# Optimization experiments

Hardware: AMD Instinct MI355X
Metric: run time of the kernel (lower is better)

## Reference

```python
import jax, jax.numpy as jnp
import numpy as np

NUM_HEADS = 4
SPLIT_SIZE = 8  # idx == 1 -> H_sp = H, W_sp = split_size (vertical stripe windows)


def setup_inputs() -> dict:
    key = jax.random.key(0)
    k1, k2, k3 = jax.random.split(key, 3)
    temp = jax.random.normal(k1, (16, 3, 128, 64, 64), dtype=jnp.float32)
    conv_w = jax.random.normal(k2, (128, 1, 3, 3), dtype=jnp.float32) * 0.1  # depthwise LePE conv
    conv_b = jax.random.normal(k3, (128,), dtype=jnp.float32) * 0.1
    return {"temp": temp, "conv_w": conv_w, "conv_b": conv_b}


def reference(temp, conv_w, conv_b):
    B, _, C, H, W = temp.shape
    H_sp, W_sp = H, SPLIT_SIZE          # idx == 1 cross-shaped window
    # H % H_sp == 0 and W % W_sp == 0 -> F.pad amounts are zero here
    nH, nW = H // H_sp, W // W_sp
    L = H_sp * W_sp                     # tokens per window
    hd = C // NUM_HEADS
    scale = hd ** -0.5

    q, k, v = temp[:, 0], temp[:, 1], temp[:, 2]  # each [B, C, H, W]

    def im2cswin(x):
        # img2windows: B C H W -> (B*nH*nW, L, C) then split heads -> (Bw, nh, L, hd)
        x = x.reshape(B, C, nH, H_sp, nW, W_sp).transpose(0, 2, 4, 3, 5, 1)
        x = x.reshape(-1, L, NUM_HEADS, hd).transpose(0, 2, 1, 3)
        return x

    qw = im2cswin(q) * scale            # (Bw, nh, L, hd)
    kw = im2cswin(k)

    # get_rpe: window-partition v as images, depthwise 3x3 conv for LePE
    vimg = v.reshape(B, C, nH, H_sp, nW, W_sp).transpose(0, 2, 4, 1, 3, 5)
    vimg = vimg.reshape(-1, C, H_sp, W_sp)  # (Bw, C, H_sp, W_sp)
    rpe = jax.lax.conv_general_dilated(
        vimg, conv_w, window_strides=(1, 1), padding="SAME",
        dimension_numbers=("NCHW", "OIHW", "NCHW"), feature_group_count=C,
    ) + conv_b[None, :, None, None]
    rpe = rpe.reshape(-1, NUM_HEADS, hd, L).transpose(0, 1, 3, 2)  # (Bw, nh, L, hd)
    vw = vimg.reshape(-1, NUM_HEADS, hd, L).transpose(0, 1, 3, 2)

    attn = jax.nn.softmax(jnp.einsum("wnld,wnmd->wnlm", qw, kw), axis=-1)
    out = jnp.einsum("wnlm,wnmd->wnld", attn, vw) + rpe  # (Bw, nh, L, hd)

    out = out.transpose(0, 2, 1, 3).reshape(-1, L, C)    # (Bw, L, C)
    # windows2img: (Bw, L, C) -> (B, H, W, C)
    out = out.reshape(B, nH, nW, H_sp, W_sp, C).transpose(0, 1, 3, 2, 4, 5)
    out = out.reshape(B, H, W, C)
    return out.reshape(B, H * W, C)
```

## Files before the change

### kernel.cpp

```cpp
#include <hip/hip_runtime.h>

typedef __attribute__((ext_vector_type(8))) short short8;
typedef __attribute__((ext_vector_type(2))) float float2_t;
typedef __attribute__((ext_vector_type(4))) float float4_t;
typedef __attribute__((ext_vector_type(4))) int int4_t;
typedef __attribute__((ext_vector_type(2))) unsigned uint2_t;

#define CH_STRIDE 4096
#define IMG_STRIDE 524288
#define HW 4096
#define V520 520

static __device__ __forceinline__ short f2b(float x) {
    unsigned u = __builtin_bit_cast(unsigned, x);
    u = (u + 0x7fffu + ((u >> 16) & 1u)) >> 16;
    return (short)u;
}
static __device__ __forceinline__ float bitsf(unsigned u) { return __builtin_bit_cast(float, u); }
static __device__ __forceinline__ unsigned bitsu(float f) { return __builtin_bit_cast(unsigned, f); }

__global__ __launch_bounds__(1024) void cswin_fused(
    const float* __restrict__ temp, const float* __restrict__ cw,
    const float* __restrict__ cb, float* __restrict__ out)
{
    __shared__ short Kc[64 * 40];
    __shared__ short Vt[32 * V520];

    int bx = blockIdx.x;
    int nw = bx >> 6;
    int r  = bx & 63;
    int b  = r >> 2;
    int n  = r & 3;

    int t    = threadIdx.x;
    int wv   = t >> 6;
    int lane = t & 63;
    int mr   = lane & 15;
    int q    = lane >> 4;

    const float* tq = temp + (size_t)b * 3 * IMG_STRIDE + (size_t)(n * 32) * CH_STRIDE + nw * 8;
    const float* tk = tq + IMG_STRIDE;
    const float* tv = tk + IMG_STRIDE;

    int row0 = wv * 32;
    const float qscale = 0.2550348889072310f;

    short8 Qf[2];
    #pragma unroll
    for (int qt = 0; qt < 2; ++qt) {
        int l = row0 + qt * 16 + mr;
        int sp = (l >> 3) * 64 + (l & 7);
        short8 f;
        #pragma unroll
        for (int j = 0; j < 8; ++j)
            f[j] = f2b(tq[(q * 8 + j) * CH_STRIDE + sp] * qscale);
        Qf[qt] = f;
    }

    float4_t zero4 = {0.f, 0.f, 0.f, 0.f};
    float4_t acc[2][2];
    #pragma unroll
    for (int dt = 0; dt < 2; ++dt)
        #pragma unroll
        for (int qt = 0; qt < 2; ++qt)
            acc[dt][qt] = zero4;
    float lsum[2] = {0.f, 0.f};

    int ld  = t >> 5;
    int seg = t & 31;
    const float* tkld = tk + (size_t)ld * CH_STRIDE;
    const float* tvld = tv + (size_t)ld * CH_STRIDE;

    float kx[2], vx[2];
    #pragma unroll
    for (int i = 0; i < 2; ++i) {
        int lb = seg + 32 * i;
        int sp = (lb >> 3) * 64 + (lb & 7);
        kx[i] = tkld[sp]; vx[i] = tvld[sp];
    }
    {
        #pragma unroll
        for (int i = 0; i < 2; ++i) {
            int kl = seg + 32 * i;
            Kc[kl * 40 + ld] = f2b(kx[i]);
            Vt[ld * V520 + kl] = f2b(vx[i]);
        }
    }
    #pragma unroll
    for (int i = 0; i < 2; ++i) {
        int lb = 64 + seg + 32 * i;
        int sp = (lb >> 3) * 64 + (lb & 7);
        kx[i] = tkld[sp]; vx[i] = tvld[sp];
    }

    #pragma unroll 1
    for (int ch = 0; ch < 8; ++ch) {
        __syncthreads();

        #pragma unroll
        for (int g = 0; g < 2; ++g) {
            short8 KaA = *reinterpret_cast<const short8*>(&Kc[((2 * g) * 16 + mr) * 40 + q * 8]);
            short8 KaB = *reinterpret_cast<const short8*>(&Kc[((2 * g + 1) * 16 + mr) * 40 + q * 8]);
            unsigned pa0[2], pa1[2], pb0[2], pb1[2];
            #pragma unroll
            for (int qt = 0; qt < 2; ++qt) {
                float4_t sA = __builtin_amdgcn_mfma_f32_16x16x32_bf16(KaA, Qf[qt], zero4, 0, 0, 0);
                float4_t sB = __builtin_amdgcn_mfma_f32_16x16x32_bf16(KaB, Qf[qt], zero4, 0, 0, 0);
                float eA0 = __builtin_amdgcn_exp2f(sA.x), eA1 = __builtin_amdgcn_exp2f(sA.y);
                float eA2 = __builtin_amdgcn_exp2f(sA.z), eA3 = __builtin_amdgcn_exp2f(sA.w);
                float eB0 = __builtin_amdgcn_exp2f(sB.x), eB1 = __builtin_amdgcn_exp2f(sB.y);
                float eB2 = __builtin_amdgcn_exp2f(sB.z), eB3 = __builtin_amdgcn_exp2f(sB.w);
                lsum[qt] += ((eA0 + eA1) + (eA2 + eA3)) + ((eB0 + eB1) + (eB2 + eB3));
                pa0[qt] = __builtin_amdgcn_perm(bitsu(eA1), bitsu(eA0), 0x07060302u);
                pa1[qt] = __builtin_amdgcn_perm(bitsu(eA3), bitsu(eA2), 0x07060302u);
                pb0[qt] = __builtin_amdgcn_perm(bitsu(eB1), bitsu(eB0), 0x07060302u);
                pb1[qt] = __builtin_amdgcn_perm(bitsu(eB3), bitsu(eB2), 0x07060302u);
            }
            int base = ch * 64 + g * 32 + q * 8;
            short8 Va0 = *reinterpret_cast<const short8*>(&Vt[mr * V520 + base]);
            short8 Va1 = *reinterpret_cast<const short8*>(&Vt[(16 + mr) * V520 + base]);
            #pragma unroll
            for (int qt = 0; qt < 2; ++qt) {
                uint2_t re = __builtin_amdgcn_permlane32_swap(pa0[qt], pb0[qt], 0, 0);
                uint2_t we = __builtin_amdgcn_permlane16_swap(re.x, re.y, 0, 0);
                uint2_t ro = __builtin_amdgcn_permlane32_swap(pa1[qt], pb1[qt], 0, 0);
                uint2_t wo = __builtin_amdgcn_permlane16_swap(ro.x, ro.y, 0, 0);
                int4_t pi = { (int)we.x, (int)wo.x, (int)we.y, (int)wo.y };
                short8 Pb = __builtin_bit_cast(short8, pi);
                acc[0][qt] = __builtin_amdgcn_mfma_f32_16x16x32_bf16(Va0, Pb, acc[0][qt], 0, 0, 0);
                acc[1][qt] = __builtin_amdgcn_mfma_f32_16x16x32_bf16(Va1, Pb, acc[1][qt], 0, 0, 0);
            }
        }

        if (ch < 7) {
            __syncthreads();
            #pragma unroll
            for (int i = 0; i < 2; ++i) {
                int kl = seg + 32 * i;
                Kc[kl * 40 + ld] = f2b(kx[i]);
                Vt[ld * V520 + (ch + 1) * 64 + kl] = f2b(vx[i]);
            }
            if (ch < 6) {
                #pragma unroll
                for (int i = 0; i < 2; ++i) {
                    int lb = (ch + 2) * 64 + seg + 32 * i;
                    int sp = (lb >> 3) * 64 + (lb & 7);
                    kx[i] = tkld[sp]; vx[i] = tvld[sp];
                }
            }
        }
    }

    float inv[2];
    #pragma unroll
    for (int qt = 0; qt < 2; ++qt) {
        float v = lsum[qt];
        v += __shfl_xor(v, 16);
        v += __shfl_xor(v, 32);
        inv[qt] = 1.0f / v;
    }

    float* outb = out + (size_t)b * HW * 128 + nw * 8 * 128 + n * 32;
    #pragma unroll
    for (int qt = 0; qt < 2; ++qt) {
        int l = row0 + qt * 16 + mr;
        size_t basep = (size_t)((l >> 3) * 64 + (l & 7)) * 128;
        #pragma unroll
        for (int dt = 0; dt < 2; ++dt) {
            float4_t o = acc[dt][qt] * inv[qt];
            *reinterpret_cast<float4_t*>(outb + basep + dt * 16 + q * 4) = o;
        }
    }

    __syncthreads();

    int c2 = (t & 15) * 2;
    int h  = t >> 4;
    float2_t outv[8];
    #pragma unroll
    for (int cc = 0; cc < 2; ++cc) {
        int c = c2 + cc;
        float w9[9];
        #pragma unroll
        for (int i = 0; i < 9; ++i) w9[i] = cw[(n * 32 + c) * 9 + i];
        float bias = cb[n * 32 + c];
        float rv[3][8];
        #pragma unroll
        for (int rr = 0; rr < 3; ++rr) {
            int hh = h - 1 + rr;
            if (hh >= 0 && hh < 64) {
                short8 u = *reinterpret_cast<const short8*>(&Vt[c * V520 + hh * 8]);
                #pragma unroll
                for (int j = 0; j < 8; ++j)
                    rv[rr][j] = bitsf(((unsigned)(unsigned short)u[j]) << 16);
            } else {
                #pragma unroll
                for (int j = 0; j < 8; ++j) rv[rr][j] = 0.f;
            }
        }
        #pragma unroll
        for (int w = 0; w < 8; ++w) {
            float o = bias;
            #pragma unroll
            for (int rr = 0; rr < 3; ++rr) {
                if (w > 0) o += rv[rr][w - 1] * w9[rr * 3 + 0];
                o += rv[rr][w] * w9[rr * 3 + 1];
                if (w < 7) o += rv[rr][w + 1] * w9[rr * 3 + 2];
            }
            outv[w][cc] = o;
        }
    }
    #pragma unroll
    for (int w = 0; w < 8; ++w) {
        size_t off = (size_t)h * 8192 + w * 128 + c2;
        float2_t cur = *reinterpret_cast<const float2_t*>(outb + off);
        cur += outv[w];
        *reinterpret_cast<float2_t*>(outb + off) = cur;
    }
}

extern "C" void kernel_launch(void* const* d_in, const int* in_sizes, int n_in,
                              void* d_out, int out_size, void* d_ws, size_t ws_size,
                              hipStream_t stream) {
    const float* temp = (const float*)d_in[0];
    const float* cw   = (const float*)d_in[1];
    const float* cb   = (const float*)d_in[2];
    float* out = (float*)d_out;
    hipLaunchKernelGGL(cswin_fused, dim3(512), dim3(1024), 0, stream, temp, cw, cb, out);
}
```

Measured before the change: 186.9 us.

## Stage full K/V window in LDS with vectorized loads, drop per-chunk syncs

Result: slower. 197.4 us (+5.6%).

```diff
diff --git a/kernel.cpp b/kernel.cpp
--- a/kernel.cpp
+++ b/kernel.cpp
@@ -1,6 +1,7 @@
 #include <hip/hip_runtime.h>
 
 typedef __attribute__((ext_vector_type(8))) short short8;
+typedef __attribute__((ext_vector_type(4))) short short4_t;
 typedef __attribute__((ext_vector_type(2))) float float2_t;
 typedef __attribute__((ext_vector_type(4))) float float4_t;
 typedef __attribute__((ext_vector_type(4))) int int4_t;
@@ -10,6 +11,7 @@
 #define IMG_STRIDE 524288
 #define HW 4096
 #define V520 520
+#define K40 40
 
 static __device__ __forceinline__ short f2b(float x) {
     unsigned u = __builtin_bit_cast(unsigned, x);
@@ -23,7 +25,7 @@
     const float* __restrict__ temp, const float* __restrict__ cw,
     const float* __restrict__ cb, float* __restrict__ out)
 {
-    __shared__ short Kc[64 * 40];
+    __shared__ short Kt[512 * K40];
     __shared__ short Vt[32 * V520];
 
     int bx = blockIdx.x;
@@ -45,6 +47,20 @@
     int row0 = wv * 32;
     const float qscale = 0.2550348889072310f;
 
+    int ld = t >> 5;
+    int qs = t & 31;
+    const float* tkld = tk + (size_t)ld * CH_STRIDE;
+    const float* tvld = tv + (size_t)ld * CH_STRIDE;
+
+    float4_t kq[4], vq[4];
+    #pragma unroll
+    for (int i = 0; i < 4; ++i) {
+        int qq = qs + 32 * i;
+        int sp = (qq >> 1) * 64 + 4 * (qq & 1);
+        kq[i] = *reinterpret_cast<const float4_t*>(tkld + sp);
+        vq[i] = *reinterpret_cast<const float4_t*>(tvld + sp);
+    }
+
     short8 Qf[2];
     #pragma unroll
     for (int qt = 0; qt < 2; ++qt) {
@@ -57,6 +73,18 @@
         Qf[qt] = f;
     }
 
+    #pragma unroll
+    for (int i = 0; i < 4; ++i) {
+        int qq = qs + 32 * i;
+        int k0 = 4 * qq;
+        Kt[(k0 + 0) * K40 + ld] = f2b(kq[i].x);
+        Kt[(k0 + 1) * K40 + ld] = f2b(kq[i].y);
+        Kt[(k0 + 2) * K40 + ld] = f2b(kq[i].z);
+        Kt[(k0 + 3) * K40 + ld] = f2b(kq[i].w);
+        short4_t vs = { f2b(vq[i].x), f2b(vq[i].y), f2b(vq[i].z), f2b(vq[i].w) };
+        *reinterpret_cast<short4_t*>(&Vt[ld * V520 + k0]) = vs;
+    }
+
     float4_t zero4 = {0.f, 0.f, 0.f, 0.f};
     float4_t acc[2][2];
     #pragma unroll
@@ -66,41 +94,17 @@
             acc[dt][qt] = zero4;
     float lsum[2] = {0.f, 0.f};
 
-    int ld  = t >> 5;
-    int seg = t & 31;
-    const float* tkld = tk + (size_t)ld * CH_STRIDE;
-    const float* tvld = tv + (size_t)ld * CH_STRIDE;
-
-    float kx[2], vx[2];
-    #pragma unroll
-    for (int i = 0; i < 2; ++i) {
-        int lb = seg + 32 * i;
-        int sp = (lb >> 3) * 64 + (lb & 7);
-        kx[i] = tkld[sp]; vx[i] = tvld[sp];
-    }
-    {
-        #pragma unroll
-        for (int i = 0; i < 2; ++i) {
-            int kl = seg + 32 * i;
-            Kc[kl * 40 + ld] = f2b(kx[i]);
-            Vt[ld * V520 + kl] = f2b(vx[i]);
-        }
-    }
-    #pragma unroll
-    for (int i = 0; i < 2; ++i) {
-        int lb = 64 + seg + 32 * i;
-        int sp = (lb >> 3) * 64 + (lb & 7);
-        kx[i] = tkld[sp]; vx[i] = tvld[sp];
-    }
-
-    #pragma unroll 1
-    for (int ch = 0; ch < 8; ++ch) {
-        __syncthreads();
+    __syncthreads();
+
+    #pragma unroll 2
+    for (int cc = 0; cc < 8; ++cc) {
+        int ch = (cc + wv) & 7;
+        const short* Kr = &Kt[ch * 64 * K40];
 
         #pragma unroll
         for (int g = 0; g < 2; ++g) {
-            short8 KaA = *reinterpret_cast<const short8*>(&Kc[((2 * g) * 16 + mr) * 40 + q * 8]);
-            short8 KaB = *reinterpret_cast<const short8*>(&Kc[((2 * g + 1) * 16 + mr) * 40 + q * 8]);
+            short8 KaA = *reinterpret_cast<const short8*>(&Kr[((2 * g) * 16 + mr) * K40 + q * 8]);
+            short8 KaB = *reinterpret_cast<const short8*>(&Kr[((2 * g + 1) * 16 + mr) * K40 + q * 8]);
             unsigned pa0[2], pa1[2], pb0[2], pb1[2];
             #pragma unroll
             for (int qt = 0; qt < 2; ++qt) {
@@ -131,24 +135,6 @@
                 acc[1][qt] = __builtin_amdgcn_mfma_f32_16x16x32_bf16(Va1, Pb, acc[1][qt], 0, 0, 0);
             }
         }
-
-        if (ch < 7) {
-            __syncthreads();
-            #pragma unroll
-            for (int i = 0; i < 2; ++i) {
-                int kl = seg + 32 * i;
-                Kc[kl * 40 + ld] = f2b(kx[i]);
-                Vt[ld * V520 + (ch + 1) * 64 + kl] = f2b(vx[i]);
-            }
-            if (ch < 6) {
-                #pragma unroll
-                for (int i = 0; i < 2; ++i) {
-                    int lb = (ch + 2) * 64 + seg + 32 * i;
-                    int sp = (lb >> 3) * 64 + (lb & 7);
-                    kx[i] = tkld[sp]; vx[i] = tvld[sp];
-                }
-            }
-        }
     }
 
     float inv[2];
```

## Split each window-head across four 256-thread blocks with per-block query slices

Applied to the files above, without the earlier changes.

New measurement: 200.5 us. 7.3% more time.

```diff
diff --git a/kernel.cpp b/kernel.cpp
--- a/kernel.cpp
+++ b/kernel.cpp
@@ -1,6 +1,7 @@
 #include <hip/hip_runtime.h>
 
 typedef __attribute__((ext_vector_type(8))) short short8;
+typedef __attribute__((ext_vector_type(4))) short short4_t;
 typedef __attribute__((ext_vector_type(2))) float float2_t;
 typedef __attribute__((ext_vector_type(4))) float float4_t;
 typedef __attribute__((ext_vector_type(4))) int int4_t;
@@ -9,7 +10,8 @@
 #define CH_STRIDE 4096
 #define IMG_STRIDE 524288
 #define HW 4096
-#define V520 520
+#define VC72 72
+#define VT152 152
 
 static __device__ __forceinline__ short f2b(float x) {
     unsigned u = __builtin_bit_cast(unsigned, x);
@@ -19,18 +21,19 @@
 static __device__ __forceinline__ float bitsf(unsigned u) { return __builtin_bit_cast(float, u); }
 static __device__ __forceinline__ unsigned bitsu(float f) { return __builtin_bit_cast(unsigned, f); }
 
-__global__ __launch_bounds__(1024) void cswin_fused(
+__global__ __launch_bounds__(256) void cswin_fused(
     const float* __restrict__ temp, const float* __restrict__ cw,
     const float* __restrict__ cb, float* __restrict__ out)
 {
     __shared__ short Kc[64 * 40];
-    __shared__ short Vt[32 * V520];
+    __shared__ short Vc[32 * VC72];
+    __shared__ short Vtc[32 * VT152];
 
     int bx = blockIdx.x;
-    int nw = bx >> 6;
-    int r  = bx & 63;
-    int b  = r >> 2;
-    int n  = r & 3;
+    int qq = bx >> 9;
+    int nw = (bx >> 6) & 7;
+    int b  = (bx >> 2) & 15;
+    int n  = bx & 3;
 
     int t    = threadIdx.x;
     int wv   = t >> 6;
@@ -38,11 +41,13 @@
     int mr   = lane & 15;
     int q    = lane >> 4;
 
+    int kb0 = qq * 128 - 8;
+
     const float* tq = temp + (size_t)b * 3 * IMG_STRIDE + (size_t)(n * 32) * CH_STRIDE + nw * 8;
     const float* tk = tq + IMG_STRIDE;
     const float* tv = tk + IMG_STRIDE;
 
-    int row0 = wv * 32;
+    int row0 = qq * 128 + wv * 32;
     const float qscale = 0.2550348889072310f;
 
     short8 Qf[2];
@@ -66,32 +71,39 @@
             acc[dt][qt] = zero4;
     float lsum[2] = {0.f, 0.f};
 
-    int ld  = t >> 5;
-    int seg = t & 31;
+    int ld = t >> 3;
+    int qs = t & 7;
     const float* tkld = tk + (size_t)ld * CH_STRIDE;
     const float* tvld = tv + (size_t)ld * CH_STRIDE;
-
-    float kx[2], vx[2];
-    #pragma unroll
-    for (int i = 0; i < 2; ++i) {
-        int lb = seg + 32 * i;
-        int sp = (lb >> 3) * 64 + (lb & 7);
-        kx[i] = tkld[sp]; vx[i] = tvld[sp];
-    }
+    int kl0a = 4 * qs, kl0b = 4 * (qs + 8);
+    int spba = (kl0a >> 3) * 64 + (kl0a & 7);
+    int spbb = (kl0b >> 3) * 64 + (kl0b & 7);
+
+    float4_t kq[2], vq[2];
+    kq[0] = *reinterpret_cast<const float4_t*>(tkld + spba);
+    kq[1] = *reinterpret_cast<const float4_t*>(tkld + spbb);
+    vq[0] = *reinterpret_cast<const float4_t*>(tvld + spba);
+    vq[1] = *reinterpret_cast<const float4_t*>(tvld + spbb);
     {
         #pragma unroll
         for (int i = 0; i < 2; ++i) {
-            int kl = seg + 32 * i;
-            Kc[kl * 40 + ld] = f2b(kx[i]);
-            Vt[ld * V520 + kl] = f2b(vx[i]);
-        }
-    }
-    #pragma unroll
-    for (int i = 0; i < 2; ++i) {
-        int lb = 64 + seg + 32 * i;
-        int sp = (lb >> 3) * 64 + (lb & 7);
-        kx[i] = tkld[sp]; vx[i] = tvld[sp];
-    }
+            int kl = i ? kl0b : kl0a;
+            float4_t kk = kq[i], vv = vq[i];
+            Kc[(kl + 0) * 40 + ld] = f2b(kk.x);
+            Kc[(kl + 1) * 40 + ld] = f2b(kk.y);
+            Kc[(kl + 2) * 40 + ld] = f2b(kk.z);
+            Kc[(kl + 3) * 40 + ld] = f2b(kk.w);
+            short4_t vs = { f2b(vv.x), f2b(vv.y), f2b(vv.z), f2b(vv.w) };
+            *reinterpret_cast<short4_t*>(&Vc[ld * VC72 + kl]) = vs;
+            int rk = kl - kb0;
+            if (rk >= 0 && rk < 144)
+                *reinterpret_cast<short4_t*>(&Vtc[ld * VT152 + rk]) = vs;
+        }
+    }
+    kq[0] = *reinterpret_cast<const float4_t*>(tkld + 512 + spba);
+    kq[1] = *reinterpret_cast<const float4_t*>(tkld + 512 + spbb);
+    vq[0] = *reinterpret_cast<const float4_t*>(tvld + 512 + spba);
+    vq[1] = *reinterpret_cast<const float4_t*>(tvld + 512 + spbb);
 
     #pragma unroll 1
     for (int ch = 0; ch < 8; ++ch) {
@@ -116,9 +128,9 @@
                 pb0[qt] = __builtin_amdgcn_perm(bitsu(eB1), bitsu(eB0), 0x07060302u);
                 pb1[qt] = __builtin_amdgcn_perm(bitsu(eB3), bitsu(eB2), 0x07060302u);
             }
-            int base = ch * 64 + g * 32 + q * 8;
-            short8 Va0 = *reinterpret_cast<const short8*>(&Vt[mr * V520 + base]);
-            short8 Va1 = *reinterpret_cast<const short8*>(&Vt[(16 + mr) * V520 + base]);
+            int base = g * 32 + q * 8;
+            short8 Va0 = *reinterpret_cast<const short8*>(&Vc[mr * VC72 + base]);
+            short8 Va1 = *reinterpret_cast<const short8*>(&Vc[(16 + mr) * VC72 + base]);
             #pragma unroll
             for (int qt = 0; qt < 2; ++qt) {
                 uint2_t re = __builtin_amdgcn_permlane32_swap(pa0[qt], pb0[qt], 0, 0);
@@ -136,17 +148,24 @@
             __syncthreads();
             #pragma unroll
             for (int i = 0; i < 2; ++i) {
-                int kl = seg + 32 * i;
-                Kc[kl * 40 + ld] = f2b(kx[i]);
-                Vt[ld * V520 + (ch + 1) * 64 + kl] = f2b(vx[i]);
+                int kl = i ? kl0b : kl0a;
+                float4_t kk = kq[i], vv = vq[i];
+                Kc[(kl + 0) * 40 + ld] = f2b(kk.x);
+                Kc[(kl + 1) * 40 + ld] = f2b(kk.y);
+                Kc[(kl + 2) * 40 + ld] = f2b(kk.z);
+                Kc[(kl + 3) * 40 + ld] = f2b(kk.w);
+                short4_t vs = { f2b(vv.x), f2b(vv.y), f2b(vv.z), f2b(vv.w) };
+                *reinterpret_cast<short4_t*>(&Vc[ld * VC72 + kl]) = vs;
+                int rk = (ch + 1) * 64 + kl - kb0;
+                if (rk >= 0 && rk < 144)
+                    *reinterpret_cast<short4_t*>(&Vtc[ld * VT152 + rk]) = vs;
             }
             if (ch < 6) {
-                #pragma unroll
-                for (int i = 0; i < 2; ++i) {
-                    int lb = (ch + 2) * 64 + seg + 32 * i;
-                    int sp = (lb >> 3) * 64 + (lb & 7);
-                    kx[i] = tkld[sp]; vx[i] = tvld[sp];
-                }
+                int off = (ch + 2) * 512;
+                kq[0] = *reinterpret_cast<const float4_t*>(tkld + off + spba);
+                kq[1] = *reinterpret_cast<const float4_t*>(tkld + off + spbb);
+                vq[0] = *reinterpret_cast<const float4_t*>(tvld + off + spba);
+                vq[1] = *reinterpret_cast<const float4_t*>(tvld + off + spbb);
             }
         }
     }
@@ -175,7 +194,7 @@
     __syncthreads();
 
     int c2 = (t & 15) * 2;
-    int h  = t >> 4;
+    int h  = qq * 16 + (t >> 4);
     float2_t outv[8];
     #pragma unroll
     for (int cc = 0; cc < 2; ++cc) {
@@ -189,7 +208,7 @@
         for (int rr = 0; rr < 3; ++rr) {
             int hh = h - 1 + rr;
             if (hh >= 0 && hh < 64) {
-                short8 u = *reinterpret_cast<const short8*>(&Vt[c * V520 + hh * 8]);
+                short8 u = *reinterpret_cast<const short8*>(&Vtc[c * VT152 + (hh * 8 - kb0)]);
                 #pragma unroll
                 for (int j = 0; j < 8; ++j)
                     rv[rr][j] = bitsf(((unsigned)(unsigned short)u[j]) << 16);
@@ -226,5 +245,5 @@
     const float* cw   = (const float*)d_in[1];
     const float* cb   = (const float*)d_in[2];
     float* out = (float*)d_out;
-    hipLaunchKernelGGL(cswin_fused, dim3(512), dim3(1024), 0, stream, temp, cw, cb, out);
+    hipLaunchKernelGGL(cswin_fused, dim3(2048), dim3(256), 0, stream, temp, cw, cb, out);
 }
```
